# Kernel optimization log

Hardware: AMD Instinct MI355X
Metric: run time of the kernel (lower is better)

Reference implementation:

```python
import jax, jax.numpy as jnp
import numpy as np

N_ATOMS = 100000
N_EDGES = 200000  # paired: edge 2i and 2i+1 are reverses of each other
N_MOLS = 4096
D_V, D_E, D_H = 133, 14, 512
DEPTH = 3
BN_EPS = 1e-5


def setup_inputs() -> dict:
    key = jax.random.key(0)
    ks = jax.random.split(key, 10)
    V = jax.random.normal(ks[0], (N_ATOMS, D_V), dtype=jnp.float32)
    E = jax.random.normal(ks[1], (N_EDGES, D_E), dtype=jnp.float32)
    # paired directed edges: (src,dst) at 2i, (dst,src) at 2i+1 -> rev index is i^1
    half = N_EDGES // 2
    s = jax.random.randint(ks[2], (half,), 0, N_ATOMS, dtype=jnp.int32)
    d = jax.random.randint(ks[3], (half,), 0, N_ATOMS, dtype=jnp.int32)
    edge_src = jnp.stack([s, d], axis=1).reshape(-1)
    edge_dst = jnp.stack([d, s], axis=1).reshape(-1)
    batch = jnp.sort(jax.random.randint(ks[4], (N_ATOMS,), 0, N_MOLS, dtype=jnp.int32))
    sc = 0.02
    W_i = jax.random.normal(ks[5], (D_V + D_E, D_H), dtype=jnp.float32) * sc
    W_h = jax.random.normal(ks[6], (D_H, D_H), dtype=jnp.float32) * sc
    W_o = jax.random.normal(ks[7], (D_V + D_H, D_H), dtype=jnp.float32) * sc
    b_o = jnp.zeros((D_H,), dtype=jnp.float32)
    gamma = jnp.ones((D_H,), dtype=jnp.float32)
    beta = jnp.zeros((D_H,), dtype=jnp.float32)
    return {"V": V, "E": E, "edge_src": edge_src, "edge_dst": edge_dst,
            "batch": batch, "W_i": W_i, "W_h": W_h, "W_o": W_o, "b_o": b_o,
            "gamma": gamma, "beta": beta}


def reference(V, E, edge_src, edge_dst, batch, W_i, W_h, W_o, b_o, gamma, beta):
    n_atoms = V.shape[0]
    n_edges = E.shape[0]
    rev = jnp.arange(n_edges, dtype=jnp.int32) ^ 1  # reverse-bond index

    # --- BondMessagePassing (chemprop v2) ---
    # initialize: H_0 = W_i([V[src] ; E]), H = relu(H_0)
    H0 = jnp.concatenate([V[edge_src], E], axis=1) @ W_i  # [n_edges, d_h]
    H = jax.nn.relu(H0)
    for _ in range(DEPTH - 1):
        # message: sum of incoming edge states at dst node, gathered at src,
        # minus the reverse edge's own state
        M_node = jax.ops.segment_sum(H, edge_dst, num_segments=n_atoms)
        M = M_node[edge_src] - H[rev]
        # update: H = relu(H_0 + W_h(M)) (dropout = 0)
        H = jax.nn.relu(H0 + M @ W_h)
    # finalize: aggregate edges to nodes, H_v = relu(W_o([V ; M_v]))
    M_v = jax.ops.segment_sum(H, edge_dst, num_segments=n_atoms)
    H_v = jax.nn.relu(jnp.concatenate([V, M_v], axis=1) @ W_o + b_o)  # [n_atoms, d_h]

    # --- MeanAggregation over batch ids ---
    sums = jax.ops.segment_sum(H_v, batch, num_segments=N_MOLS)
    counts = jax.ops.segment_sum(jnp.ones((n_atoms,), H_v.dtype), batch, num_segments=N_MOLS)
    h_mol = sums / jnp.maximum(counts, 1.0)[:, None]  # [n_mols, d_h]

    # --- BatchNorm1d (training mode: batch statistics, biased variance) ---
    mu = h_mol.mean(axis=0)
    var = h_mol.var(axis=0)
    return (h_mol - mu) * jax.lax.rsqrt(var + BN_EPS) * gamma + beta
```

## Files before the change

### kernel.cpp

```cpp
#include <hip/hip_runtime.h>

typedef _Float16 f16;
typedef _Float16 half8 __attribute__((ext_vector_type(8)));
typedef _Float16 half4v __attribute__((ext_vector_type(4)));
typedef float f32x4 __attribute__((ext_vector_type(4)));

#define N_ATOMS 100000
#define N_EDGES 200000
#define N_MOLS  4096
#define D_V 133
#define D_E 14
#define D_H 512
#define KC  672
#define KSE 21
#define LDA 40

__global__ void wt_build_swz(const float* __restrict__ W1, int r1,
                             const float* __restrict__ W2, int r2,
                             f16* __restrict__ WtS) {
    int gid = blockIdx.x * blockDim.x + threadIdx.x;
    if (gid >= D_H * KC) return;
    int n = gid / KC;
    int k = gid - n * KC;
    float x = 0.f;
    if (k < r1) x = W1[k * D_H + n];
    else if (k < r1 + r2) x = W2[(k - r1) * D_H + n];
    const int dst = ((((n >> 4) * KSE + (k >> 5)) << 6) + (((k >> 3) & 3) << 4) + (n & 15)) * 8 + (k & 7);
    WtS[dst] = (f16)x;
}

__global__ void csr_hist(const int* __restrict__ edst, int* __restrict__ cnt) {
    int e = blockIdx.x * blockDim.x + threadIdx.x;
    if (e < N_EDGES) atomicAdd(&cnt[edst[e]], 1);
}

__global__ __launch_bounds__(1024) void csr_scan(const int* __restrict__ cnt,
                                                 int* __restrict__ off, int* __restrict__ pos) {
    __shared__ int sums[1024];
    const int tid = threadIdx.x;
    const int lo = tid * 98;
    const int hi = min(lo + 98, N_ATOMS);
    int s = 0;
    for (int i = lo; i < hi; ++i) s += cnt[i];
    sums[tid] = s;
    __syncthreads();
    for (int d = 1; d < 1024; d <<= 1) {
        int v = (tid >= d) ? sums[tid - d] : 0;
        __syncthreads();
        sums[tid] += v;
        __syncthreads();
    }
    int run = sums[tid] - s;
    for (int i = lo; i < hi; ++i) { off[i] = run; pos[i] = run; run += cnt[i]; }
    if (tid == 1023) off[N_ATOMS] = run;
}

__global__ void csr_scatter(const int* __restrict__ edst, int* __restrict__ pos,
                            int* __restrict__ eid) {
    int e = blockIdx.x * blockDim.x + threadIdx.x;
    if (e < N_EDGES) {
        int idx = atomicAdd(&pos[edst[e]], 1);
        eid[idx] = e;
    }
}

template<bool F16M>
__global__ __launch_bounds__(512) void seg_csr(
    const f16* __restrict__ H, const int* __restrict__ off, const int* __restrict__ eid,
    void* __restrict__ MnOut, float* __restrict__ Msc)
{
    const int n = blockIdx.x * 8 + (threadIdx.x >> 6);
    const int lane = threadIdx.x & 63;
    const int j0 = off[n], j1 = off[n + 1];
    float acc[8];
    #pragma unroll
    for (int k = 0; k < 8; ++k) acc[k] = 0.f;
    for (int j = j0; j < j1; ++j) {
        const int e = eid[j];
        const half8 h = *reinterpret_cast<const half8*>(&H[e * D_H + lane * 8]);
        #pragma unroll
        for (int k = 0; k < 8; ++k) acc[k] += (float)h[k];
    }
    if (F16M) {
        half8 o;
        #pragma unroll
        for (int k = 0; k < 8; ++k) o[k] = (f16)acc[k];
        *reinterpret_cast<half8*>(&((f16*)MnOut)[n * D_H + lane * 8]) = o;
    } else {
        float m = 0.f;
        #pragma unroll
        for (int k = 0; k < 8; ++k) m = fmaxf(m, fabsf(acc[k]));
        m = fmaxf(m, __shfl_xor(m, 1));
        m = fmaxf(m, __shfl_xor(m, 2));
        m = fmaxf(m, 1e-20f);
        const float s = m * (1.f / 127.f);
        const float inv_s = 127.f / m;
        if ((lane & 3) == 0) Msc[n * 16 + (lane >> 2)] = s;
        int q[8];
        #pragma unroll
        for (int k = 0; k < 8; ++k) q[k] = __float2int_rn(acc[k] * inv_s);
        uint2 o;
        o.x = (q[0] & 0xff) | ((q[1] & 0xff) << 8) | ((q[2] & 0xff) << 16) | ((unsigned)(q[3] & 0xff) << 24);
        o.y = (q[4] & 0xff) | ((q[5] & 0xff) << 8) | ((q[6] & 0xff) << 16) | ((unsigned)(q[7] & 0xff) << 24);
        *reinterpret_cast<uint2*>(&((unsigned int*)MnOut)[n * 128 + lane * 2]) = o;
    }
}

template<bool F16M>
__global__ __launch_bounds__(512) void gemm_pass(
    const float* __restrict__ V, const float* __restrict__ E,
    const int* __restrict__ esrc, const void* __restrict__ Mn,
    const float* __restrict__ Msc,
    f16* __restrict__ Ha, const f16* __restrict__ WtS, int ks_begin)
{
    __shared__ __align__(16) f16 Al[64 * LDA];
    const int tid = threadIdx.x;
    const int rowblk = blockIdx.x << 6;
    const int srow = tid >> 3;
    const int skk  = (tid & 7) << 2;
    const int e_s  = rowblk + srow;
    const int sv   = esrc[e_s];
    const int rev  = e_s ^ 1;
    const int lane = tid & 63;
    const int quad = lane >> 4;
    const int m16  = lane & 15;
    const int colbase = (tid >> 6) << 6;
    const int cb0 = (tid >> 6) << 2;
    const f16* WtL = WtS + lane * 8;

    f32x4 acc[4][4];
    #pragma unroll
    for (int a = 0; a < 4; ++a)
    #pragma unroll
    for (int b = 0; b < 4; ++b)
    #pragma unroll
    for (int r = 0; r < 4; ++r) acc[a][b][r] = 0.f;

    char4 pq; float ps; half4v pm; half4v ph; float pv[4];
    auto issue = [&](int ks) {
        const int k0 = ks << 5;
        if (k0 < D_H) {
            if (F16M) {
                pm = *reinterpret_cast<const half4v*>(&((const f16*)Mn)[sv * D_H + k0 + skk]);
            } else {
                pq = *reinterpret_cast<const char4*>(&((const char*)Mn)[sv * D_H + k0 + skk]);
                ps = Msc[sv * 16 + (k0 >> 5)];
            }
            ph = *reinterpret_cast<const half4v*>(&Ha[rev * D_H + k0 + skk]);
        } else {
            #pragma unroll
            for (int j = 0; j < 4; ++j) {
                const int kk = k0 + skk + j - D_H;
                float x = 0.f;
                if (kk < D_V) x = V[sv * D_V + kk];
                else if (kk < D_V + D_E) x = E[e_s * D_E + (kk - D_V)];
                pv[j] = x;
            }
        }
    };

    issue(ks_begin);
    for (int ks = ks_begin; ks < KSE; ++ks) {
        const int k0 = ks << 5;
        half4v w;
        if (k0 < D_H) {
            if (F16M) {
                w = pm - ph;
            } else {
                w[0] = (f16)((float)pq.x * ps - (float)ph[0]);
                w[1] = (f16)((float)pq.y * ps - (float)ph[1]);
                w[2] = (f16)((float)pq.z * ps - (float)ph[2]);
                w[3] = (f16)((float)pq.w * ps - (float)ph[3]);
            }
        } else {
            w[0] = (f16)pv[0]; w[1] = (f16)pv[1]; w[2] = (f16)pv[2]; w[3] = (f16)pv[3];
        }
        __syncthreads();
        *reinterpret_cast<half4v*>(&Al[srow * LDA + skk]) = w;
        __syncthreads();
        if (ks + 1 < KSE) issue(ks + 1);
        half8 af[4];
        #pragma unroll
        for (int rt = 0; rt < 4; ++rt)
            af[rt] = *reinterpret_cast<const half8*>(&Al[(rt * 16 + m16) * LDA + quad * 8]);
        #pragma unroll
        for (int ct = 0; ct < 4; ++ct) {
            const half8 bf = *reinterpret_cast<const half8*>(&WtL[(((cb0 + ct) * KSE + ks) << 9)]);
            #pragma unroll
            for (int rt = 0; rt < 4; ++rt)
                acc[rt][ct] = __builtin_amdgcn_mfma_f32_16x16x32_f16(af[rt], bf, acc[rt][ct], 0, 0, 0);
        }
    }

    #pragma unroll
    for (int rt = 0; rt < 4; ++rt)
    #pragma unroll
    for (int ct = 0; ct < 4; ++ct)
    #pragma unroll
    for (int r = 0; r < 4; ++r) {
        const int row = rowblk + rt * 16 + quad * 4 + r;
        const int col = colbase + ct * 16 + m16;
        Ha[row * D_H + col] = (f16)fmaxf(acc[rt][ct][r], 0.f);
    }
}

template<bool F16M>
__global__ __launch_bounds__(512) void gemm_out(
    const float* __restrict__ V, const void* __restrict__ Mn,
    const float* __restrict__ Msc, const float* __restrict__ bo,
    const f16* __restrict__ WtS, f16* __restrict__ Hv)
{
    __shared__ __align__(16) f16 Al[64 * LDA];
    __shared__ float bo_s[D_H];
    const int tid = threadIdx.x;
    const int rowblk = blockIdx.x << 6;
    bo_s[tid] = bo[tid];
    const int srow = tid >> 3;
    const int skk  = (tid & 7) << 2;
    const int arow = min(rowblk + srow, N_ATOMS - 1);
    const int lane = tid & 63;
    const int quad = lane >> 4;
    const int m16  = lane & 15;
    const int colbase = (tid >> 6) << 6;
    const int cb0 = (tid >> 6) << 2;
    const f16* WtL = WtS + lane * 8;

    f32x4 acc[4][4];
    #pragma unroll
    for (int a = 0; a < 4; ++a)
    #pragma unroll
    for (int b = 0; b < 4; ++b)
    #pragma unroll
    for (int r = 0; r < 4; ++r) acc[a][b][r] = 0.f;

    char4 pq; float ps; half4v pm; float pv[4];
    auto issue = [&](int ks) {
        const int k0 = ks << 5;
        if (k0 < D_H) {
            if (F16M) {
                pm = *reinterpret_cast<const half4v*>(&((const f16*)Mn)[arow * D_H + k0 + skk]);
            } else {
                pq = *reinterpret_cast<const char4*>(&((const char*)Mn)[arow * D_H + k0 + skk]);
                ps = Msc[arow * 16 + (k0 >> 5)];
            }
        } else {
            #pragma unroll
            for (int j = 0; j < 4; ++j) {
                const int kk = k0 + skk + j - D_H;
                pv[j] = (kk < D_V) ? V[arow * D_V + kk] : 0.f;
            }
        }
    };

    issue(0);
    for (int ks = 0; ks < KSE; ++ks) {
        const int k0 = ks << 5;
        half4v w;
        if (k0 < D_H) {
            if (F16M) {
                w = pm;
            } else {
                w[0] = (f16)((float)pq.x * ps);
                w[1] = (f16)((float)pq.y * ps);
                w[2] = (f16)((float)pq.z * ps);
                w[3] = (f16)((float)pq.w * ps);
            }
        } else {
            w[0] = (f16)pv[0]; w[1] = (f16)pv[1]; w[2] = (f16)pv[2]; w[3] = (f16)pv[3];
        }
        __syncthreads();
        *reinterpret_cast<half4v*>(&Al[srow * LDA + skk]) = w;
        __syncthreads();
        if (ks + 1 < KSE) issue(ks + 1);
        half8 af[4];
        #pragma unroll
        for (int rt = 0; rt < 4; ++rt)
            af[rt] = *reinterpret_cast<const half8*>(&Al[(rt * 16 + m16) * LDA + quad * 8]);
        #pragma unroll
        for (int ct = 0; ct < 4; ++ct) {
            const half8 bf = *reinterpret_cast<const half8*>(&WtL[(((cb0 + ct) * KSE + ks) << 9)]);
            #pragma unroll
            for (int rt = 0; rt < 4; ++rt)
                acc[rt][ct] = __builtin_amdgcn_mfma_f32_16x16x32_f16(af[rt], bf, acc[rt][ct], 0, 0, 0);
        }
    }

    #pragma unroll
    for (int rt = 0; rt < 4; ++rt)
    #pragma unroll
    for (int ct = 0; ct < 4; ++ct)
    #pragma unroll
    for (int r = 0; r < 4; ++r) {
        const int row = rowblk + rt * 16 + quad * 4 + r;
        if (row < N_ATOMS) {
            const int col = colbase + ct * 16 + m16;
            Hv[row * D_H + col] = (f16)fmaxf(acc[rt][ct][r] + bo_s[col], 0.f);
        }
    }
}

__global__ __launch_bounds__(512) void mol_mean(
    const f16* __restrict__ Hv, const int* __restrict__ batch, float* __restrict__ mean)
{
    const int m = blockIdx.x;
    __shared__ int sh[2];
    if (threadIdx.x == 0) {
        int lo = 0, hi = N_ATOMS;
        while (lo < hi) { int mid = (lo + hi) >> 1; if (batch[mid] < m) lo = mid + 1; else hi = mid; }
        sh[0] = lo;
        int lo2 = lo; hi = N_ATOMS;
        while (lo2 < hi) { int mid = (lo2 + hi) >> 1; if (batch[mid] < m + 1) lo2 = mid + 1; else hi = mid; }
        sh[1] = lo2;
    }
    __syncthreads();
    const int a0 = sh[0], a1 = sh[1];
    float acc = 0.f;
    for (int a = a0; a < a1; ++a) acc += (float)Hv[(size_t)a * D_H + threadIdx.x];
    mean[m * D_H + threadIdx.x] = acc / (float)max(a1 - a0, 1);
}

__global__ __launch_bounds__(256) void bn_stats(
    const float* __restrict__ mean_in, const float* __restrict__ gamma,
    const float* __restrict__ beta, float* __restrict__ An, float* __restrict__ Bn)
{
    const int n = blockIdx.x;
    const int tid = threadIdx.x;
    float s = 0.f, s2 = 0.f;
    for (int m = tid; m < N_MOLS; m += 256) {
        float h = mean_in[m * D_H + n];
        s += h; s2 += h * h;
    }
    for (int off = 32; off > 0; off >>= 1) {
        s  += __shfl_down(s, off);
        s2 += __shfl_down(s2, off);
    }
    __shared__ float sh[8];
    const int wave = tid >> 6, lane = tid & 63;
    if (lane == 0) { sh[wave] = s; sh[4 + wave] = s2; }
    __syncthreads();
    if (tid == 0) {
        float S  = sh[0] + sh[1] + sh[2] + sh[3];
        float S2 = sh[4] + sh[5] + sh[6] + sh[7];
        float mu = S / (float)N_MOLS;
        float var = fmaxf(S2 / (float)N_MOLS - mu * mu, 0.f);
        float sc = rsqrtf(var + 1e-5f) * gamma[n];
        An[n] = sc;
        Bn[n] = beta[n] - mu * sc;
    }
}

__global__ void bn_apply(const float* __restrict__ mean_in,
                         const float* __restrict__ An, const float* __restrict__ Bn,
                         float* __restrict__ out)
{
    int gid = blockIdx.x * blockDim.x + threadIdx.x;
    int n = gid & 511;
    out[gid] = mean_in[gid] * An[n] + Bn[n];
}

extern "C" void kernel_launch(void* const* d_in, const int* in_sizes, int n_in,
                              void* d_out, int out_size, void* d_ws, size_t ws_size,
                              hipStream_t stream)
{
    (void)in_sizes; (void)n_in; (void)out_size;
    const float* V     = (const float*)d_in[0];
    const float* E     = (const float*)d_in[1];
    const int*   esrc  = (const int*)d_in[2];
    const int*   edst  = (const int*)d_in[3];
    const int*   batch = (const int*)d_in[4];
    const float* Wi    = (const float*)d_in[5];
    const float* Wh    = (const float*)d_in[6];
    const float* Wo    = (const float*)d_in[7];
    const float* bo    = (const float*)d_in[8];
    const float* gam   = (const float*)d_in[9];
    const float* bet   = (const float*)d_in[10];
    float* out = (float*)d_out;

    char* ws = (char*)d_ws;
    f16*   WtC  = (f16*)(ws + 0);
    f16*   WtO  = (f16*)(ws + 688128);
    int*   off  = (int*)(ws + 1376256);
    int*   eid  = (int*)(ws + 1776384);
    int*   cnt  = (int*)(ws + 2576384);
    float* An   = (float*)(ws + 2992768);
    float* Bn   = (float*)(ws + 2994816);
    f16*   Ha   = (f16*)(ws + 2996864);
    void*  Mn   = (void*)(ws + 207796864);
    float* Msc  = (float*)(ws + 258996864);
    f16*   Hv   = Ha;
    float* mean = out;

    const bool f16m = ws_size >= 310196864ULL;

    wt_build_swz<<<(D_H * KC + 255) / 256, 256, 0, stream>>>(Wh, D_H, Wi, D_V + D_E, WtC);
    wt_build_swz<<<(D_H * KC + 255) / 256, 256, 0, stream>>>(Wo + D_V * D_H, D_H, Wo, D_V, WtO);

    hipMemsetAsync(cnt, 0, 400000, stream);
    csr_hist<<<(N_EDGES + 511) / 512, 512, 0, stream>>>(edst, cnt);
    csr_scan<<<1, 1024, 0, stream>>>(cnt, off, cnt);
    csr_scatter<<<(N_EDGES + 511) / 512, 512, 0, stream>>>(edst, cnt, eid);

    if (f16m) {
        gemm_pass<true><<<N_EDGES / 64, 512, 0, stream>>>(V, E, esrc, Mn, Msc, Ha, WtC, 16);
        for (int it = 0; it < 2; ++it) {
            seg_csr<true><<<N_ATOMS / 8, 512, 0, stream>>>(Ha, off, eid, Mn, Msc);
            gemm_pass<true><<<N_EDGES / 64, 512, 0, stream>>>(V, E, esrc, Mn, Msc, Ha, WtC, 0);
        }
        seg_csr<true><<<N_ATOMS / 8, 512, 0, stream>>>(Ha, off, eid, Mn, Msc);
        gemm_out<true><<<(N_ATOMS + 63) / 64, 512, 0, stream>>>(V, Mn, Msc, bo, WtO, Hv);
    } else {
        gemm_pass<false><<<N_EDGES / 64, 512, 0, stream>>>(V, E, esrc, Mn, Msc, Ha, WtC, 16);
        for (int it = 0; it < 2; ++it) {
            seg_csr<false><<<N_ATOMS / 8, 512, 0, stream>>>(Ha, off, eid, Mn, Msc);
            gemm_pass<false><<<N_EDGES / 64, 512, 0, stream>>>(V, E, esrc, Mn, Msc, Ha, WtC, 0);
        }
        seg_csr<false><<<N_ATOMS / 8, 512, 0, stream>>>(Ha, off, eid, Mn, Msc);
        gemm_out<false><<<(N_ATOMS + 63) / 64, 512, 0, stream>>>(V, Mn, Msc, bo, WtO, Hv);
    }

    mol_mean<<<N_MOLS, 512, 0, stream>>>(Hv, batch, mean);
    bn_stats<<<D_H, 256, 0, stream>>>(mean, gam, bet, An, Bn);
    bn_apply<<<(N_MOLS * D_H) / 256, 256, 0, stream>>>(mean, An, Bn, out);
}
```

Measured before the change: 1.520 ms.

## Double-buffer LDS and deepen global prefetch in GEMM kernels; vectorize CSR scan

```diff
diff --git a/kernel.cpp b/kernel.cpp
--- a/kernel.cpp
+++ b/kernel.cpp
@@ -38,10 +38,13 @@
                                                  int* __restrict__ off, int* __restrict__ pos) {
     __shared__ int sums[1024];
     const int tid = threadIdx.x;
-    const int lo = tid * 98;
-    const int hi = min(lo + 98, N_ATOMS);
+    const int lo = tid * 100;
     int s = 0;
-    for (int i = lo; i < hi; ++i) s += cnt[i];
+    if (lo < N_ATOMS) {
+        const int4* c4 = reinterpret_cast<const int4*>(cnt + lo);
+        #pragma unroll
+        for (int i = 0; i < 25; ++i) { int4 v = c4[i]; s += v.x + v.y + v.z + v.w; }
+    }
     sums[tid] = s;
     __syncthreads();
     for (int d = 1; d < 1024; d <<= 1) {
@@ -51,7 +54,17 @@
         __syncthreads();
     }
     int run = sums[tid] - s;
-    for (int i = lo; i < hi; ++i) { off[i] = run; pos[i] = run; run += cnt[i]; }
+    if (lo < N_ATOMS) {
+        const int4* c4 = reinterpret_cast<const int4*>(cnt + lo);
+        for (int i = 0; i < 25; ++i) {
+            int4 v = c4[i];
+            const int b = lo + i * 4;
+            off[b]     = run; pos[b]     = run; run += v.x;
+            off[b + 1] = run; pos[b + 1] = run; run += v.y;
+            off[b + 2] = run; pos[b + 2] = run; run += v.z;
+            off[b + 3] = run; pos[b + 3] = run; run += v.w;
+        }
+    }
     if (tid == 1023) off[N_ATOMS] = run;
 }
 
@@ -75,11 +88,13 @@
     float acc[8];
     #pragma unroll
     for (int k = 0; k < 8; ++k) acc[k] = 0.f;
+    int e_cur = (j0 < j1) ? eid[j0] : 0;
     for (int j = j0; j < j1; ++j) {
-        const int e = eid[j];
-        const half8 h = *reinterpret_cast<const half8*>(&H[e * D_H + lane * 8]);
+        const int e_nxt = (j + 1 < j1) ? eid[j + 1] : 0;
+        const half8 h = *reinterpret_cast<const half8*>(&H[e_cur * D_H + lane * 8]);
         #pragma unroll
         for (int k = 0; k < 8; ++k) acc[k] += (float)h[k];
+        e_cur = e_nxt;
     }
     if (F16M) {
         half8 o;
@@ -106,14 +121,14 @@
     }
 }
 
-template<bool F16M>
-__global__ __launch_bounds__(512) void gemm_pass(
+template<bool F16M, int KS0>
+__global__ __launch_bounds__(512, 4) void gemm_pass(
     const float* __restrict__ V, const float* __restrict__ E,
     const int* __restrict__ esrc, const void* __restrict__ Mn,
     const float* __restrict__ Msc,
-    f16* __restrict__ Ha, const f16* __restrict__ WtS, int ks_begin)
-{
-    __shared__ __align__(16) f16 Al[64 * LDA];
+    f16* __restrict__ Ha, const f16* __restrict__ WtS)
+{
+    __shared__ __align__(16) f16 Al[2][64 * LDA];
     const int tid = threadIdx.x;
     const int rowblk = blockIdx.x << 6;
     const int srow = tid >> 3;
@@ -136,53 +151,78 @@
     #pragma unroll
     for (int r = 0; r < 4; ++r) acc[a][b][r] = 0.f;
 
-    char4 pq; float ps; half4v pm; half4v ph; float pv[4];
-    auto issue = [&](int ks) {
-        const int k0 = ks << 5;
-        if (k0 < D_H) {
-            if (F16M) {
-                pm = *reinterpret_cast<const half4v*>(&((const f16*)Mn)[sv * D_H + k0 + skk]);
-            } else {
-                pq = *reinterpret_cast<const char4*>(&((const char*)Mn)[sv * D_H + k0 + skk]);
-                ps = Msc[sv * 16 + (k0 >> 5)];
-            }
-            ph = *reinterpret_cast<const half4v*>(&Ha[rev * D_H + k0 + skk]);
-        } else {
-            #pragma unroll
-            for (int j = 0; j < 4; ++j) {
-                const int kk = k0 + skk + j - D_H;
-                float x = 0.f;
-                if (kk < D_V) x = V[sv * D_V + kk];
-                else if (kk < D_V + D_E) x = E[e_s * D_E + (kk - D_V)];
-                pv[j] = x;
-            }
-        }
-    };
-
-    issue(ks_begin);
-    for (int ks = ks_begin; ks < KSE; ++ks) {
-        const int k0 = ks << 5;
+    char4 pq0, pq1, pq2; float ps0, ps1, ps2;
+    half4v pm0, pm1, pm2; half4v ph0, ph1, ph2;
+    float pv0[4], pv1[4], pv2[4];
+
+#define GP_ISSUE(S, KSV) do {                                                        \
+    const int ks_i_ = (KSV);                                                         \
+    if (ks_i_ < KSE) {                                                               \
+        const int k0_ = ks_i_ << 5;                                                  \
+        if (k0_ < D_H) {                                                             \
+            if (F16M) {                                                              \
+                pm##S = *reinterpret_cast<const half4v*>(&((const f16*)Mn)[sv * D_H + k0_ + skk]); \
+            } else {                                                                 \
+                pq##S = *reinterpret_cast<const char4*>(&((const char*)Mn)[sv * D_H + k0_ + skk]); \
+                ps##S = Msc[sv * 16 + (k0_ >> 5)];                                   \
+            }                                                                        \
+            ph##S = *reinterpret_cast<const half4v*>(&Ha[rev * D_H + k0_ + skk]);    \
+        } else {                                                                     \
+            const int kb_ = k0_ + skk - D_H;                                         \
+            pv##S[0] = (kb_ + 0 < D_V) ? V[sv * D_V + kb_ + 0] : ((kb_ + 0 < D_V + D_E) ? E[e_s * D_E + kb_ + 0 - D_V] : 0.f); \
+            pv##S[1] = (kb_ + 1 < D_V) ? V[sv * D_V + kb_ + 1] : ((kb_ + 1 < D_V + D_E) ? E[e_s * D_E + kb_ + 1 - D_V] : 0.f); \
+            pv##S[2] = (kb_ + 2 < D_V) ? V[sv * D_V + kb_ + 2] : ((kb_ + 2 < D_V + D_E) ? E[e_s * D_E + kb_ + 2 - D_V] : 0.f); \
+            pv##S[3] = (kb_ + 3 < D_V) ? V[sv * D_V + kb_ + 3] : ((kb_ + 3 < D_V + D_E) ? E[e_s * D_E + kb_ + 3 - D_V] : 0.f); \
+        }                                                                            \
+    }                                                                                \
+} while (0)
+
+#define GP_MAKEW(S, KSV, W) do {                                                     \
+    const int k0_ = (KSV) << 5;                                                      \
+    if (k0_ < D_H) {                                                                 \
+        if (F16M) { W = pm##S - ph##S; }                                             \
+        else {                                                                       \
+            W[0] = (f16)((float)pq##S.x * ps##S - (float)ph##S[0]);                  \
+            W[1] = (f16)((float)pq##S.y * ps##S - (float)ph##S[1]);                  \
+            W[2] = (f16)((float)pq##S.z * ps##S - (float)ph##S[2]);                  \
+            W[3] = (f16)((float)pq##S.w * ps##S - (float)ph##S[3]);                  \
+        }                                                                            \
+    } else {                                                                         \
+        W[0] = (f16)pv##S[0]; W[1] = (f16)pv##S[1];                                  \
+        W[2] = (f16)pv##S[2]; W[3] = (f16)pv##S[3];                                  \
+    }                                                                                \
+} while (0)
+
+    GP_ISSUE(0, KS0);
+    GP_ISSUE(1, KS0 + 1);
+    GP_ISSUE(2, KS0 + 2);
+    {
         half4v w;
-        if (k0 < D_H) {
-            if (F16M) {
-                w = pm - ph;
-            } else {
-                w[0] = (f16)((float)pq.x * ps - (float)ph[0]);
-                w[1] = (f16)((float)pq.y * ps - (float)ph[1]);
-                w[2] = (f16)((float)pq.z * ps - (float)ph[2]);
-                w[3] = (f16)((float)pq.w * ps - (float)ph[3]);
-            }
-        } else {
-            w[0] = (f16)pv[0]; w[1] = (f16)pv[1]; w[2] = (f16)pv[2]; w[3] = (f16)pv[3];
-        }
-        __syncthreads();
-        *reinterpret_cast<half4v*>(&Al[srow * LDA + skk]) = w;
-        __syncthreads();
-        if (ks + 1 < KSE) issue(ks + 1);
+        GP_MAKEW(0, KS0, w);
+        *reinterpret_cast<half4v*>(&Al[0][srow * LDA + skk]) = w;
+        GP_ISSUE(0, KS0 + 3);
+    }
+    __syncthreads();
+
+    #pragma unroll
+    for (int ks = KS0; ks < KSE; ++ks) {
+        const int i = ks - KS0;
+        const int cur = i & 1;
+        if (ks + 1 < KSE) {
+            const int sl = (i + 1) % 3;
+            half4v w;
+            if (sl == 0)      GP_MAKEW(0, ks + 1, w);
+            else if (sl == 1) GP_MAKEW(1, ks + 1, w);
+            else              GP_MAKEW(2, ks + 1, w);
+            *reinterpret_cast<half4v*>(&Al[cur ^ 1][srow * LDA + skk]) = w;
+            if (sl == 0)      GP_ISSUE(0, ks + 4);
+            else if (sl == 1) GP_ISSUE(1, ks + 4);
+            else              GP_ISSUE(2, ks + 4);
+        }
         half8 af[4];
         #pragma unroll
         for (int rt = 0; rt < 4; ++rt)
-            af[rt] = *reinterpret_cast<const half8*>(&Al[(rt * 16 + m16) * LDA + quad * 8]);
+            af[rt] = *reinterpret_cast<const half8*>(&Al[cur][(rt * 16 + m16) * LDA + quad * 8]);
         #pragma unroll
         for (int ct = 0; ct < 4; ++ct) {
             const half8 bf = *reinterpret_cast<const half8*>(&WtL[(((cb0 + ct) * KSE + ks) << 9)]);
@@ -190,7 +230,10 @@
             for (int rt = 0; rt < 4; ++rt)
                 acc[rt][ct] = __builtin_amdgcn_mfma_f32_16x16x32_f16(af[rt], bf, acc[rt][ct], 0, 0, 0);
         }
-    }
+        __syncthreads();
+    }
+#undef GP_ISSUE
+#undef GP_MAKEW
 
     #pragma unroll
     for (int rt = 0; rt < 4; ++rt)
@@ -205,12 +248,12 @@
 }
 
 template<bool F16M>
-__global__ __launch_bounds__(512) void gemm_out(
+__global__ __launch_bounds__(512, 4) void gemm_out(
     const float* __restrict__ V, const void* __restrict__ Mn,
     const float* __restrict__ Msc, const float* __restrict__ bo,
     const f16* __restrict__ WtS, f16* __restrict__ Hv)
 {
-    __shared__ __align__(16) f16 Al[64 * LDA];
+    __shared__ __align__(16) f16 Al[2][64 * LDA];
     __shared__ float bo_s[D_H];
     const int tid = threadIdx.x;
     const int rowblk = blockIdx.x << 6;
@@ -233,49 +276,76 @@
     #pragma unroll
     for (int r = 0; r < 4; ++r) acc[a][b][r] = 0.f;
 
-    char4 pq; float ps; half4v pm; float pv[4];
-    auto issue = [&](int ks) {
-        const int k0 = ks << 5;
-        if (k0 < D_H) {
-            if (F16M) {
-                pm = *reinterpret_cast<const half4v*>(&((const f16*)Mn)[arow * D_H + k0 + skk]);
-            } else {
-                pq = *reinterpret_cast<const char4*>(&((const char*)Mn)[arow * D_H + k0 + skk]);
-                ps = Msc[arow * 16 + (k0 >> 5)];
-            }
-        } else {
-            #pragma unroll
-            for (int j = 0; j < 4; ++j) {
-                const int kk = k0 + skk + j - D_H;
-                pv[j] = (kk < D_V) ? V[arow * D_V + kk] : 0.f;
-            }
-        }
-    };
-
-    issue(0);
+    char4 pq0, pq1, pq2; float ps0, ps1, ps2;
+    half4v pm0, pm1, pm2;
+    float pv0[4], pv1[4], pv2[4];
+
+#define GO_ISSUE(S, KSV) do {                                                        \
+    const int ks_i_ = (KSV);                                                         \
+    if (ks_i_ < KSE) {                                                               \
+        const int k0_ = ks_i_ << 5;                                                  \
+        if (k0_ < D_H) {                                                             \
+            if (F16M) {                                                              \
+                pm##S = *reinterpret_cast<const half4v*>(&((const f16*)Mn)[arow * D_H + k0_ + skk]); \
+            } else {                                                                 \
+                pq##S = *reinterpret_cast<const char4*>(&((const char*)Mn)[arow * D_H + k0_ + skk]); \
+                ps##S = Msc[arow * 16 + (k0_ >> 5)];                                 \
+            }                                                                        \
+        } else {                                                                     \
+            const int kb_ = k0_ + skk - D_H;                                         \
+            pv##S[0] = (kb_ + 0 < D_V) ? V[arow * D_V + kb_ + 0] : 0.f;              \
+            pv##S[1] = (kb_ + 1 < D_V) ? V[arow * D_V + kb_ + 1] : 0.f;              \
+            pv##S[2] = (kb_ + 2 < D_V) ? V[arow * D_V + kb_ + 2] : 0.f;              \
+            pv##S[3] = (kb_ + 3 < D_V) ? V[arow * D_V + kb_ + 3] : 0.f;              \
+        }                                                                            \
+    }                                                                                \
+} while (0)
+
+#define GO_MAKEW(S, KSV, W) do {                                                     \
+    const int k0_ = (KSV) << 5;                                                      \
+    if (k0_ < D_H) {                                                                 \
+        if (F16M) { W = pm##S; }                                                     \
+        else {                                                                       \
+            W[0] = (f16)((float)pq##S.x * ps##S);                                    \
+            W[1] = (f16)((float)pq##S.y * ps##S);                                    \
+            W[2] = (f16)((float)pq##S.z * ps##S);                                    \
+            W[3] = (f16)((float)pq##S.w * ps##S);                                    \
+        }                                                                            \
+    } else {                                                                         \
+        W[0] = (f16)pv##S[0]; W[1] = (f16)pv##S[1];                                  \
+        W[2] = (f16)pv##S[2]; W[3] = (f16)pv##S[3];                                  \
+    }                                                                                \
+} while (0)
+
+    GO_ISSUE(0, 0);
+    GO_ISSUE(1, 1);
+    GO_ISSUE(2, 2);
+    {
+        half4v w;
+        GO_MAKEW(0, 0, w);
+        *reinterpret_cast<half4v*>(&Al[0][srow * LDA + skk]) = w;
+        GO_ISSUE(0, 3);
+    }
+    __syncthreads();
+
+    #pragma unroll
     for (int ks = 0; ks < KSE; ++ks) {
-        const int k0 = ks << 5;
-        half4v w;
-        if (k0 < D_H) {
-            if (F16M) {
-                w = pm;
-            } else {
-                w[0] = (f16)((float)pq.x * ps);
-                w[1] = (f16)((float)pq.y * ps);
-                w[2] = (f16)((float)pq.z * ps);
-                w[3] = (f16)((float)pq.w * ps);
-            }
-        } else {
-            w[0] = (f16)pv[0]; w[1] = (f16)pv[1]; w[2] = (f16)pv[2]; w[3] = (f16)pv[3];
-        }
-        __syncthreads();
-        *reinterpret_cast<half4v*>(&Al[srow * LDA + skk]) = w;
-        __syncthreads();
-        if (ks + 1 < KSE) issue(ks + 1);
+        const int cur = ks & 1;
+        if (ks + 1 < KSE) {
+            const int sl = (ks + 1) % 3;
+            half4v w;
+            if (sl == 0)      GO_MAKEW(0, ks + 1, w);
+            else if (sl == 1) GO_MAKEW(1, ks + 1, w);
+            else              GO_MAKEW(2, ks + 1, w);
+            *reinterpret_cast<half4v*>(&Al[cur ^ 1][srow * LDA + skk]) = w;
+            if (sl == 0)      GO_ISSUE(0, ks + 4);
+            else if (sl == 1) GO_ISSUE(1, ks + 4);
+            else              GO_ISSUE(2, ks + 4);
+        }
         half8 af[4];
         #pragma unroll
         for (int rt = 0; rt < 4; ++rt)
-            af[rt] = *reinterpret_cast<const half8*>(&Al[(rt * 16 + m16) * LDA + quad * 8]);
+            af[rt] = *reinterpret_cast<const half8*>(&Al[cur][(rt * 16 + m16) * LDA + quad * 8]);
         #pragma unroll
         for (int ct = 0; ct < 4; ++ct) {
             const half8 bf = *reinterpret_cast<const half8*>(&WtL[(((cb0 + ct) * KSE + ks) << 9)]);
@@ -283,7 +353,10 @@
             for (int rt = 0; rt < 4; ++rt)
                 acc[rt][ct] = __builtin_amdgcn_mfma_f32_16x16x32_f16(af[rt], bf, acc[rt][ct], 0, 0, 0);
         }
-    }
+        __syncthreads();
+    }
+#undef GO_ISSUE
+#undef GO_MAKEW
 
     #pragma unroll
     for (int rt = 0; rt < 4; ++rt)
@@ -401,18 +474,18 @@
     csr_scatter<<<(N_EDGES + 511) / 512, 512, 0, stream>>>(edst, cnt, eid);
 
     if (f16m) {
-        gemm_pass<true><<<N_EDGES / 64, 512, 0, stream>>>(V, E, esrc, Mn, Msc, Ha, WtC, 16);
+        gemm_pass<true, 16><<<N_EDGES / 64, 512, 0, stream>>>(V, E, esrc, Mn, Msc, Ha, WtC);
         for (int it = 0; it < 2; ++it) {
             seg_csr<true><<<N_ATOMS / 8, 512, 0, stream>>>(Ha, off, eid, Mn, Msc);
-            gemm_pass<true><<<N_EDGES / 64, 512, 0, stream>>>(V, E, esrc, Mn, Msc, Ha, WtC, 0);
+            gemm_pass<true, 0><<<N_EDGES / 64, 512, 0, stream>>>(V, E, esrc, Mn, Msc, Ha, WtC);
         }
         seg_csr<true><<<N_ATOMS / 8, 512, 0, stream>>>(Ha, off, eid, Mn, Msc);
         gemm_out<true><<<(N_ATOMS + 63) / 64, 512, 0, stream>>>(V, Mn, Msc, bo, WtO, Hv);
     } else {
-        gemm_pass<false><<<N_EDGES / 64, 512, 0, stream>>>(V, E, esrc, Mn, Msc, Ha, WtC, 16);
+        gemm_pass<false, 16><<<N_EDGES / 64, 512, 0, stream>>>(V, E, esrc, Mn, Msc, Ha, WtC);
         for (int it = 0; it < 2; ++it) {
             seg_csr<false><<<N_ATOMS / 8, 512, 0, stream>>>(Ha, off, eid, Mn, Msc);
-            gemm_pass<false><<<N_EDGES / 64, 512, 0, stream>>>(V, E, esrc, Mn, Msc, Ha, WtC, 0);
+            gemm_pass<false, 0><<<N_EDGES / 64, 512, 0, stream>>>(V, E, esrc, Mn, Msc, Ha, WtC);
         }
         seg_csr<false><<<N_ATOMS / 8, 512, 0, stream>>>(Ha, off, eid, Mn, Msc);
         gemm_out<false><<<(N_ATOMS + 63) / 64, 512, 0, stream>>>(V, Mn, Msc, bo, WtO, Hv);
```

Measured after the change: 1.440 ms. 1.06x faster.
